# Kernel tuning notes

Measured on AMD Instinct MI355X. Metric: run time of the kernel, lower is better.

## Reference

```python
import jax, jax.numpy as jnp
import numpy as np
from jax import lax

NUM_HEADS = 8
BN_EPS = 1e-5


def setup_inputs() -> dict:
    key = jax.random.key(0)
    ks = jax.random.split(key, 11)
    B, C, H, W = 4, 256, 48, 48
    return {
        "Vx": jax.random.normal(ks[0], (B, C, H, W), jnp.float32),
        "conv_w": jax.random.normal(ks[1], (C, C, 3, 3), jnp.float32) * 0.02,
        "conv_b": jax.random.normal(ks[2], (C,), jnp.float32) * 0.02,
        "bn_gamma": jax.random.uniform(ks[3], (C,), jnp.float32, 0.5, 1.5),
        "bn_beta": jax.random.normal(ks[4], (C,), jnp.float32) * 0.02,
        "bn_mean": jax.random.normal(ks[5], (C,), jnp.float32) * 0.02,
        "bn_var": jax.random.uniform(ks[6], (C,), jnp.float32, 0.5, 1.5),
        "qkv_w": jax.random.normal(ks[7], (3 * C, C), jnp.float32) * 0.02,
        "qkv_b": jax.random.normal(ks[8], (3 * C,), jnp.float32) * 0.02,
        "proj_w": jax.random.normal(ks[9], (C, C), jnp.float32) * 0.02,
        "proj_b": jax.random.normal(ks[10], (C,), jnp.float32) * 0.02,
    }


def reference(Vx, conv_w, conv_b, bn_gamma, bn_beta, bn_mean, bn_var,
              qkv_w, qkv_b, proj_w, proj_b):
    # 3x3 conv (stride 1, pad 1) + BN (inference) + ReLU
    x = lax.conv_general_dilated(
        Vx, conv_w, window_strides=(1, 1), padding='SAME',
        dimension_numbers=('NCHW', 'OIHW', 'NCHW'))
    x = x + conv_b[None, :, None, None]
    inv = bn_gamma * lax.rsqrt(bn_var + BN_EPS)
    x = x * inv[None, :, None, None] + (bn_beta - bn_mean * inv)[None, :, None, None]
    x = jax.nn.relu(x)

    B, C, H, W = x.shape
    N = H * W
    h = NUM_HEADS
    d = C // h
    scale = float(d) ** -0.5  # (dim / num_heads) ** -0.5

    # 1x1 qkv conv == channel matmul; faithful interleaved per-head split:
    # reshape(B, h, 3d, N) then chunk along dim 2
    qkv = jnp.einsum('oc,bchw->bohw', qkv_w, x) + qkv_b[None, :, None, None]
    qkv = qkv.reshape(B, h, 3 * d, N)
    q, k, v = qkv[:, :, :d], qkv[:, :, d:2 * d], qkv[:, :, 2 * d:]

    # attn[b,h,n,m] = sum_d q[b,h,d,n] k[b,h,d,m] * scale ; softmax over m
    attn = jax.nn.softmax(jnp.einsum('bhdn,bhdm->bhnm', q, k) * scale, axis=-1)
    # out = value @ attn^T : out[b,h,e,n] = sum_m v[b,h,e,m] attn[b,h,n,m]
    out = jnp.einsum('bhem,bhnm->bhen', v, attn).reshape(B, C, H, W)

    # 1x1 proj conv
    out = jnp.einsum('oc,bchw->bohw', proj_w, out) + proj_b[None, :, None, None]
    return out
```

## Files before the change

### kernel.cpp

```cpp
#include <hip/hip_runtime.h>
#include <math.h>

#define BB 4
#define CCH 256
#define NSP 2304
#define NHEAD 8
#define DH 32

typedef __bf16 bf16x8 __attribute__((ext_vector_type(8)));
typedef float f32x16 __attribute__((ext_vector_type(16)));
typedef unsigned u32x2 __attribute__((ext_vector_type(2)));
typedef unsigned u32x4 __attribute__((ext_vector_type(4)));

static __device__ __forceinline__ unsigned cvtpk(float lo, float hi) {
  unsigned r;
  asm("v_cvt_pk_bf16_f32 %0, %1, %2" : "=v"(r) : "v"(lo), "v"(hi));
  return r;
}

#if __has_builtin(__builtin_amdgcn_exp2f)
static __device__ __forceinline__ float fexp2(float x) { return __builtin_amdgcn_exp2f(x); }
#else
static __device__ __forceinline__ float fexp2(float x) { return exp2f(x); }
#endif

#if __has_builtin(__builtin_amdgcn_rcpf)
static __device__ __forceinline__ float frcp(float x) { return __builtin_amdgcn_rcpf(x); }
#else
static __device__ __forceinline__ float frcp(float x) { return 1.f / x; }
#endif

__global__ __launch_bounds__(256) void k_xt(const float* __restrict__ Vx,
    __bf16* __restrict__ xt)
{
  __shared__ __bf16 Lt[64 * 40];
  int bid = blockIdx.x;
  const int nt = bid % 36; bid /= 36;
  const int cit = bid % 8; const int b = bid / 8;
  const int n0 = nt * 64, ci0 = cit * 32;
  const int tid = threadIdx.x;
  {
    const int ci = tid >> 3, ns = (tid & 7) * 8;
    const float* src = Vx + ((size_t)(b * CCH + ci0 + ci)) * NSP + n0 + ns;
    float4 v0 = *(const float4*)src;
    float4 v1 = *(const float4*)(src + 4);
    Lt[(ns+0)*40 + ci] = (__bf16)v0.x;  Lt[(ns+1)*40 + ci] = (__bf16)v0.y;
    Lt[(ns+2)*40 + ci] = (__bf16)v0.z;  Lt[(ns+3)*40 + ci] = (__bf16)v0.w;
    Lt[(ns+4)*40 + ci] = (__bf16)v1.x;  Lt[(ns+5)*40 + ci] = (__bf16)v1.y;
    Lt[(ns+6)*40 + ci] = (__bf16)v1.z;  Lt[(ns+7)*40 + ci] = (__bf16)v1.w;
  }
  __syncthreads();
  {
    const int n = tid >> 2, cip = (tid & 3) * 8;
    bf16x8 r = *(bf16x8*)&Lt[n * 40 + cip];
    *(bf16x8*)&xt[((size_t)b * NSP + n0 + n) * CCH + ci0 + cip] = r;
  }
}

__global__ __launch_bounds__(256) void k_wt(const float* __restrict__ cw,
    __bf16* __restrict__ wt)
{
  const int co = blockIdx.x, ci = threadIdx.x;
  const float* rd = cw + ((size_t)co * CCH + ci) * 9;
#pragma unroll
  for (int p = 0; p < 9; ++p)
    wt[((size_t)p * CCH + co) * CCH + ci] = (__bf16)rd[p];
}

#define XLP 40

__global__ __launch_bounds__(256) void k_conv_mfma(const __bf16* __restrict__ xt,
    const __bf16* __restrict__ wt,
    const float* __restrict__ cb, const float* __restrict__ g,
    const float* __restrict__ be, const float* __restrict__ mu,
    const float* __restrict__ va, __bf16* __restrict__ xq)
{
  __shared__ __bf16 Xl[300 * XLP];
  __shared__ __bf16 Wl[9 * 64 * XLP];
  __shared__ float bn[64][2];
  int bid = blockIdx.x;
  const int nt = bid % 18; bid /= 18;
  const int cot = bid % 4; const int b = bid / 4;
  const int n0 = nt * 128, co0 = cot * 64;
  const int tid = threadIdx.x;
  const int w = tid >> 6, l = tid & 63, h = l >> 5, q = l & 31;
  const int ybase0 = n0 / 48;
  const int y0b = ybase0 - 1;

  if (tid < 64) {
    const int co = co0 + tid;
    const float inv = g[co] * rsqrtf(va[co] + 1e-5f);
    bn[tid][0] = inv;
    bn[tid][1] = (cb[co] - mu[co]) * inv + be[co];
  }

  const int nabs = n0 + w * 32 + q;
  const int yab = nabs / 48, xab = nabs - yab * 48;
  const int sb = (yab - ybase0) * 50 + xab;

  const __bf16* xtb = xt + (size_t)b * NSP * CCH;

  f32x16 acc0, acc1;
#pragma unroll
  for (int r = 0; r < 16; ++r) { acc0[r] = 0.f; acc1[r] = 0.f; }

  for (int cc = 0; cc < 8; ++cc) {
    __syncthreads();
#pragma unroll
    for (int it = 0; it < 5; ++it) {
      const int v = it * 256 + tid;
      if (v < 1200) {
        const int sp = v >> 2, cip = (v & 3) * 8;
        const int r = sp / 50, xp = sp - r * 50;
        const int gy = y0b + r, gx = xp - 1;
        bf16x8 val;
#pragma unroll
        for (int j = 0; j < 8; ++j) val[j] = (__bf16)0.f;
        if ((unsigned)gy < 48u && (unsigned)gx < 48u)
          val = *(const bf16x8*)&xtb[(size_t)(gy * 48 + gx) * CCH + cc * 32 + cip];
        *(bf16x8*)&Xl[sp * XLP + cip] = val;
      }
    }
    {
      const int co = tid >> 2, cip = (tid & 3) * 8;
      const __bf16* wsrc = wt + (size_t)(co0 + co) * CCH + cc * 32 + cip;
#pragma unroll
      for (int p = 0; p < 9; ++p) {
        bf16x8 wv = *(const bf16x8*)&wsrc[(size_t)p * CCH * CCH];
        *(bf16x8*)&Wl[(p * 64 + co) * XLP + cip] = wv;
      }
    }
    __syncthreads();
#pragma unroll
    for (int p = 0; p < 9; ++p) {
      const int dy = p / 3, dx = p - 3 * (p / 3);
#pragma unroll
      for (int ks = 0; ks < 2; ++ks) {
        bf16x8 a0 = *(bf16x8*)&Wl[(p * 64 + q) * XLP + ks * 16 + 8 * h];
        bf16x8 a1 = *(bf16x8*)&Wl[(p * 64 + 32 + q) * XLP + ks * 16 + 8 * h];
        bf16x8 bf = *(bf16x8*)&Xl[(sb + dy * 50 + dx) * XLP + ks * 16 + 8 * h];
        acc0 = __builtin_amdgcn_mfma_f32_32x32x16_bf16(a0, bf, acc0, 0, 0, 0);
        acc1 = __builtin_amdgcn_mfma_f32_32x32x16_bf16(a1, bf, acc1, 0, 0, 0);
      }
    }
  }

  __bf16* op = xq + ((size_t)b * NSP + nabs) * CCH + co0;
#pragma unroll
  for (int gg = 0; gg < 4; ++gg) {
    const int cl0 = 8 * gg + 4 * h;
    float v0 = fmaxf(fmaf(acc0[4*gg+0], bn[cl0+0][0], bn[cl0+0][1]), 0.f);
    float v1 = fmaxf(fmaf(acc0[4*gg+1], bn[cl0+1][0], bn[cl0+1][1]), 0.f);
    float v2 = fmaxf(fmaf(acc0[4*gg+2], bn[cl0+2][0], bn[cl0+2][1]), 0.f);
    float v3 = fmaxf(fmaf(acc0[4*gg+3], bn[cl0+3][0], bn[cl0+3][1]), 0.f);
    u32x2 pk; pk[0] = cvtpk(v0, v1); pk[1] = cvtpk(v2, v3);
    *(u32x2*)&op[cl0] = pk;
    float w0 = fmaxf(fmaf(acc1[4*gg+0], bn[32+cl0+0][0], bn[32+cl0+0][1]), 0.f);
    float w1 = fmaxf(fmaf(acc1[4*gg+1], bn[32+cl0+1][0], bn[32+cl0+1][1]), 0.f);
    float w2 = fmaxf(fmaf(acc1[4*gg+2], bn[32+cl0+2][0], bn[32+cl0+2][1]), 0.f);
    float w3 = fmaxf(fmaf(acc1[4*gg+3], bn[32+cl0+3][0], bn[32+cl0+3][1]), 0.f);
    u32x2 qk; qk[0] = cvtpk(w0, w1); qk[1] = cvtpk(w2, w3);
    *(u32x2*)&op[32 + cl0] = qk;
  }
}

__global__ __launch_bounds__(256) void k_gemm_mfma(const __bf16* __restrict__ X,
    const float* __restrict__ Wm, const float* __restrict__ bias,
    __bf16* __restrict__ Y)
{
  __shared__ __bf16 Xl[128 * XLP];
  __shared__ __bf16 Wl[64 * XLP];
  const int tid = threadIdx.x;
  int bid = blockIdx.x;
  const int nt = bid % 18; bid /= 18;
  const int ot = bid % 12; const int b = bid / 12;
  const int o0 = ot * 64, n0 = nt * 128;
  const int w = tid >> 6, l = tid & 63, h = l >> 5, q = l & 31;

  const int xrow = tid >> 1, xcip = (tid & 1) * 16;
  const int wrow = tid >> 2, wcip = (tid & 3) * 8;
  const __bf16* Xb = X + (size_t)b * NSP * CCH + (size_t)(n0 + xrow) * CCH;

  f32x16 acc0, acc1;
#pragma unroll
  for (int r = 0; r < 16; ++r) { acc0[r] = 0.f; acc1[r] = 0.f; }

  bf16x8 xa0, xa1; float4 wa0, wa1;
  xa0 = *(const bf16x8*)&Xb[xcip];
  xa1 = *(const bf16x8*)&Xb[xcip + 8];
  wa0 = *(const float4*)&Wm[(size_t)(o0 + wrow) * CCH + wcip];
  wa1 = *(const float4*)&Wm[(size_t)(o0 + wrow) * CCH + wcip + 4];

  for (int cc = 0; cc < 8; ++cc) {
    __syncthreads();
    *(bf16x8*)&Xl[xrow * XLP + xcip]     = xa0;
    *(bf16x8*)&Xl[xrow * XLP + xcip + 8] = xa1;
    {
      bf16x8 wv;
      wv[0]=(__bf16)wa0.x; wv[1]=(__bf16)wa0.y; wv[2]=(__bf16)wa0.z; wv[3]=(__bf16)wa0.w;
      wv[4]=(__bf16)wa1.x; wv[5]=(__bf16)wa1.y; wv[6]=(__bf16)wa1.z; wv[7]=(__bf16)wa1.w;
      *(bf16x8*)&Wl[wrow * XLP + wcip] = wv;
    }
    __syncthreads();
    if (cc < 7) {
      const int c1 = (cc + 1) * 32;
      xa0 = *(const bf16x8*)&Xb[c1 + xcip];
      xa1 = *(const bf16x8*)&Xb[c1 + xcip + 8];
      wa0 = *(const float4*)&Wm[(size_t)(o0 + wrow) * CCH + c1 + wcip];
      wa1 = *(const float4*)&Wm[(size_t)(o0 + wrow) * CCH + c1 + wcip + 4];
    }
#pragma unroll
    for (int ks = 0; ks < 2; ++ks) {
      bf16x8 a0 = *(bf16x8*)&Wl[q * XLP + ks * 16 + 8 * h];
      bf16x8 a1 = *(bf16x8*)&Wl[(32 + q) * XLP + ks * 16 + 8 * h];
      bf16x8 bfr = *(bf16x8*)&Xl[(w * 32 + q) * XLP + ks * 16 + 8 * h];
      acc0 = __builtin_amdgcn_mfma_f32_32x32x16_bf16(a0, bfr, acc0, 0, 0, 0);
      acc1 = __builtin_amdgcn_mfma_f32_32x32x16_bf16(a1, bfr, acc1, 0, 0, 0);
    }
  }

  const int n = n0 + w * 32 + q;
  const float QS = 1.4426950408889634f * 0.17677669529663687f;
#pragma unroll
  for (int j = 0; j < 2; ++j) {
    const int t = 2 * ot + j;
    const int head = t / 3, comp = t - 3 * (t / 3);
    const float sc = (comp == 0) ? QS : 1.0f;
    __bf16* yb = Y + (((size_t)(b * NHEAD + head) * 3 + comp) * NSP + n) * DH;
    const f32x16& A = j ? acc1 : acc0;
#pragma unroll
    for (int gg = 0; gg < 4; ++gg) {
      const int e0 = 8 * gg + 4 * h;
      const int ob = o0 + 32 * j + e0;
      u32x2 pk;
      pk[0] = cvtpk((A[4*gg+0] + bias[ob+0]) * sc, (A[4*gg+1] + bias[ob+1]) * sc);
      pk[1] = cvtpk((A[4*gg+2] + bias[ob+2]) * sc, (A[4*gg+3] + bias[ob+3]) * sc);
      *(u32x2*)&yb[e0] = pk;
    }
  }
}

#define KLS 40
#define VLS 72
#define NSPLIT 4
#define NST 9

__global__ __launch_bounds__(256) void k_attn_mfma(const __bf16* __restrict__ qkvt,
    __bf16* __restrict__ parts, float* __restrict__ rss)
{
  __shared__ __bf16 K_lds[2][64 * KLS];
  __shared__ __bf16 Vt_lds[2][32 * VLS];
  const int tid = threadIdx.x;
  const int bid0 = blockIdx.x;
  const int bid = (bid0 & 7) * 288 + (bid0 >> 3);
  const int bh  = bid / 72;
  const int rem = bid % 72;
  const int qb  = rem >> 2;
  const int ks  = rem & 3;
  const int w  = tid >> 6;
  const int l  = tid & 63;
  const int h  = l >> 5;
  const int q  = l & 31;

  const __bf16* qg = qkvt + ((size_t)bh * 3    ) * NSP * DH;
  const __bf16* kg = qkvt + ((size_t)bh * 3 + 1) * NSP * DH;
  const __bf16* vg = qkvt + ((size_t)bh * 3 + 2) * NSP * DH;

  const int nq = qb * 128 + w * 32 + q;
  bf16x8 qf0 = *(const bf16x8*)&qg[(size_t)nq * DH + 8 * h];
  bf16x8 qf1 = *(const bf16x8*)&qg[(size_t)nq * DH + 16 + 8 * h];

  f32x16 zf;
#pragma unroll
  for (int r = 0; r < 16; ++r) zf[r] = 0.f;
  bf16x8 onesA;
#pragma unroll
  for (int j = 0; j < 8; ++j) onesA[j] = (__bf16)1.0f;

  f32x16 acc0, acc1, rsacc;
#pragma unroll
  for (int r = 0; r < 16; ++r) { acc0[r] = 0.f; acc1[r] = 0.f; rsacc[r] = 0.f; }

  const int krow = tid >> 2, kcol = (tid & 3) * 8;
  const int vrow = tid & 63, vcol = (tid >> 6) * 8;
  const int m0 = ks * (NST * 64);

  bf16x8 ka = *(const bf16x8*)&kg[(size_t)(m0 + krow) * DH + kcol];
  bf16x8 va = *(const bf16x8*)&vg[(size_t)(m0 + vrow) * DH + vcol];
  *(bf16x8*)&K_lds[0][krow * KLS + kcol] = ka;
#pragma unroll
  for (int j = 0; j < 8; ++j) Vt_lds[0][(vcol + j) * VLS + vrow] = va[j];
  ka = *(const bf16x8*)&kg[(size_t)(m0 + 64 + krow) * DH + kcol];
  va = *(const bf16x8*)&vg[(size_t)(m0 + 64 + vrow) * DH + vcol];
  __syncthreads();

  for (int s = 0; s < NST; ++s) {
    const int cur = s & 1;
    if (s + 1 < NST) {
      *(bf16x8*)&K_lds[cur ^ 1][krow * KLS + kcol] = ka;
#pragma unroll
      for (int j = 0; j < 8; ++j) Vt_lds[cur ^ 1][(vcol + j) * VLS + vrow] = va[j];
      if (s + 2 < NST) {
        const int m2 = m0 + (s + 2) * 64;
        ka = *(const bf16x8*)&kg[(size_t)(m2 + krow) * DH + kcol];
        va = *(const bf16x8*)&vg[(size_t)(m2 + vrow) * DH + vcol];
      }
    }
    __builtin_amdgcn_s_setprio(1);
#pragma unroll
    for (int kt = 0; kt < 2; ++kt) {
      bf16x8 kfr0 = *(bf16x8*)&K_lds[cur][(32*kt + q) * KLS + 8*h];
      bf16x8 kfr1 = *(bf16x8*)&K_lds[cur][(32*kt + q) * KLS + 16 + 8*h];
      f32x16 sv;
      sv = __builtin_amdgcn_mfma_f32_32x32x16_bf16(kfr0, qf0, zf, 0, 0, 0);
      sv = __builtin_amdgcn_mfma_f32_32x32x16_bf16(kfr1, qf1, sv, 0, 0, 0);
      float p[16];
#pragma unroll
      for (int r = 0; r < 16; ++r) p[r] = fexp2(sv[r]);
#pragma unroll
      for (int m = 0; m < 2; ++m) {
        unsigned pk00 = cvtpk(p[8*m+0], p[8*m+1]);
        unsigned pk01 = cvtpk(p[8*m+2], p[8*m+3]);
        unsigned pk10 = cvtpk(p[8*m+4], p[8*m+5]);
        unsigned pk11 = cvtpk(p[8*m+6], p[8*m+7]);
        asm("v_permlane32_swap_b32 %0, %1" : "+v"(pk00), "+v"(pk10));
        asm("v_permlane32_swap_b32 %0, %1" : "+v"(pk01), "+v"(pk11));
        u32x4 pw = {pk00, pk01, pk10, pk11};
        bf16x8 pfr = __builtin_bit_cast(bf16x8, pw);
        const int MT = 2*kt + m;
        bf16x8 vfr = *(bf16x8*)&Vt_lds[cur][q * VLS + 16*MT + 8*h];
        if (MT & 1) acc1 = __builtin_amdgcn_mfma_f32_32x32x16_bf16(vfr, pfr, acc1, 0, 0, 0);
        else        acc0 = __builtin_amdgcn_mfma_f32_32x32x16_bf16(vfr, pfr, acc0, 0, 0, 0);
        rsacc = __builtin_amdgcn_mfma_f32_32x32x16_bf16(onesA, pfr, rsacc, 0, 0, 0);
      }
    }
    __builtin_amdgcn_s_setprio(0);
    __syncthreads();
  }

  const int b = bh >> 3, head = bh & 7;
  __bf16* ob = parts + (size_t)ks * 2359296
             + ((size_t)b * NSP + nq) * CCH + head * DH;
#pragma unroll
  for (int gg = 0; gg < 4; ++gg) {
    const int e0 = 8 * gg + 4 * h;
    u32x2 pk;
    pk[0] = cvtpk(acc0[4*gg+0] + acc1[4*gg+0], acc0[4*gg+1] + acc1[4*gg+1]);
    pk[1] = cvtpk(acc0[4*gg+2] + acc1[4*gg+2], acc0[4*gg+3] + acc1[4*gg+3]);
    *(u32x2*)&ob[e0] = pk;
  }
  if (h == 0)
    rss[(size_t)ks * 73728 + (size_t)bh * NSP + nq] = rsacc[0];
}

__global__ __launch_bounds__(256) void k_proj_mfma(const __bf16* __restrict__ parts,
    const float* __restrict__ rss, const float* __restrict__ Wm,
    const float* __restrict__ bias, float* __restrict__ Y)
{
  __shared__ __bf16 Xl[128 * XLP];
  __shared__ __bf16 Wl[64 * XLP];
  const int tid = threadIdx.x;
  int bid = blockIdx.x;
  const int nt = bid % 18; bid /= 18;
  const int ot = bid % 4; const int b = bid / 4;
  const int o0 = ot * 64, n0 = nt * 128;
  const int w = tid >> 6, l = tid & 63, h = l >> 5, q = l & 31;

  const int xrow = tid >> 1, xcip = (tid & 1) * 16;
  const int wrow = tid >> 2, wcip = (tid & 3) * 8;
  const int nrow = n0 + xrow;
  const size_t xbase = ((size_t)b * NSP + nrow) * CCH + xcip;
  const size_t rbase = (size_t)(b * NHEAD) * NSP + nrow;

  f32x16 acc0, acc1;
#pragma unroll
  for (int r = 0; r < 16; ++r) { acc0[r] = 0.f; acc1[r] = 0.f; }

  bf16x8 pa[4], pb[4]; float rs4[4]; float4 wa0, wa1;
#pragma unroll
  for (int ksp = 0; ksp < 4; ++ksp) {
    pa[ksp] = *(const bf16x8*)&parts[(size_t)ksp * 2359296 + xbase];
    pb[ksp] = *(const bf16x8*)&parts[(size_t)ksp * 2359296 + xbase + 8];
    rs4[ksp] = rss[(size_t)ksp * 73728 + rbase];
  }
  wa0 = *(const float4*)&Wm[(size_t)(o0 + wrow) * CCH + wcip];
  wa1 = *(const float4*)&Wm[(size_t)(o0 + wrow) * CCH + wcip + 4];

  for (int cc = 0; cc < 8; ++cc) {
    __syncthreads();
    {
      const float rn = frcp(rs4[0] + rs4[1] + rs4[2] + rs4[3]);
      float s0[8], s1[8];
#pragma unroll
      for (int j = 0; j < 8; ++j) {
        s0[j] = ((float)pa[0][j] + (float)pa[1][j] + (float)pa[2][j] + (float)pa[3][j]) * rn;
        s1[j] = ((float)pb[0][j] + (float)pb[1][j] + (float)pb[2][j] + (float)pb[3][j]) * rn;
      }
      u32x4 o0v, o1v;
#pragma unroll
      for (int j = 0; j < 4; ++j) {
        o0v[j] = cvtpk(s0[2*j], s0[2*j+1]);
        o1v[j] = cvtpk(s1[2*j], s1[2*j+1]);
      }
      *(u32x4*)&Xl[xrow * XLP + xcip]     = o0v;
      *(u32x4*)&Xl[xrow * XLP + xcip + 8] = o1v;
      bf16x8 wv;
      wv[0]=(__bf16)wa0.x; wv[1]=(__bf16)wa0.y; wv[2]=(__bf16)wa0.z; wv[3]=(__bf16)wa0.w;
      wv[4]=(__bf16)wa1.x; wv[5]=(__bf16)wa1.y; wv[6]=(__bf16)wa1.z; wv[7]=(__bf16)wa1.w;
      *(bf16x8*)&Wl[wrow * XLP + wcip] = wv;
    }
    __syncthreads();
    if (cc < 7) {
      const int c1 = (cc + 1) * 32;
#pragma unroll
      for (int ksp = 0; ksp < 4; ++ksp) {
        pa[ksp] = *(const bf16x8*)&parts[(size_t)ksp * 2359296 + xbase + c1];
        pb[ksp] = *(const bf16x8*)&parts[(size_t)ksp * 2359296 + xbase + c1 + 8];
        rs4[ksp] = rss[(size_t)ksp * 73728 + (size_t)(cc + 1) * NSP + rbase];
      }
      wa0 = *(const float4*)&Wm[(size_t)(o0 + wrow) * CCH + c1 + wcip];
      wa1 = *(const float4*)&Wm[(size_t)(o0 + wrow) * CCH + c1 + wcip + 4];
    }
#pragma unroll
    for (int ks = 0; ks < 2; ++ks) {
      bf16x8 a0 = *(bf16x8*)&Wl[q * XLP + ks * 16 + 8 * h];
      bf16x8 a1 = *(bf16x8*)&Wl[(32 + q) * XLP + ks * 16 + 8 * h];
      bf16x8 bfr = *(bf16x8*)&Xl[(w * 32 + q) * XLP + ks * 16 + 8 * h];
      acc0 = __builtin_amdgcn_mfma_f32_32x32x16_bf16(a0, bfr, acc0, 0, 0, 0);
      acc1 = __builtin_amdgcn_mfma_f32_32x32x16_bf16(a1, bfr, acc1, 0, 0, 0);
    }
  }

  const int n = n0 + w * 32 + q;
#pragma unroll
  for (int j = 0; j < 2; ++j) {
    const f32x16& A = j ? acc1 : acc0;
#pragma unroll
    for (int r = 0; r < 16; ++r) {
      const int e = (r & 3) + 8 * (r >> 2) + 4 * h;
      const int o = o0 + 32 * j + e;
      Y[((size_t)b * CCH + o) * NSP + n] = A[r] + bias[o];
    }
  }
}

extern "C" void kernel_launch(void* const* d_in, const int* in_sizes, int n_in,
                              void* d_out, int out_size, void* d_ws, size_t ws_size,
                              hipStream_t stream)
{
  const float* Vx = (const float*)d_in[0];
  const float* cw = (const float*)d_in[1];
  const float* cb = (const float*)d_in[2];
  const float* g  = (const float*)d_in[3];
  const float* be = (const float*)d_in[4];
  const float* mu = (const float*)d_in[5];
  const float* va = (const float*)d_in[6];
  const float* qw = (const float*)d_in[7];
  const float* qb = (const float*)d_in[8];
  const float* pw = (const float*)d_in[9];
  const float* pb = (const float*)d_in[10];
  float* out = (float*)d_out;

  __bf16* xq    = (__bf16*)d_ws;
  __bf16* qkvt  = (__bf16*)((char*)d_ws + 4718592);
  __bf16* parts = (__bf16*)((char*)d_ws + 18874368);
  float*  rss   = (float*) ((char*)d_ws + 37748736);

  __bf16* xt = (__bf16*)d_out;
  __bf16* wt = (__bf16*)((char*)d_out + 4718592);

  k_xt<<<1152, 256, 0, stream>>>(Vx, xt);
  k_wt<<<256, 256, 0, stream>>>(cw, wt);
  k_conv_mfma<<<288, 256, 0, stream>>>(xt, wt, cb, g, be, mu, va, xq);
  k_gemm_mfma<<<4*12*18, 256, 0, stream>>>(xq, qw, qb, qkvt);
  k_attn_mfma<<<2304, 256, 0, stream>>>(qkvt, parts, rss);
  k_proj_mfma<<<4*4*18, 256, 0, stream>>>(parts, rss, pw, pb, out);
}
```

Baseline: 113.7 us.

## Merge prep kernels, shrink conv tiles, and raise attention key split to six

The input transpose and weight conversion kernels become one launch, removing a kernel boundary. The conv kernel now uses 96-pixel by 32-channel tiles with 192 threads and 768 blocks, replacing 288 blocks, to fill more compute units. Attention splits keys six ways instead of four, giving 3456 blocks, and the projection kernel sums six partial results. This adds more partial-result traffic and more redundant halo and weight loads per conv block in exchange for higher occupancy.

New measurement: 115.5 us. No clear change (+1.6%).

```diff
diff --git a/kernel.cpp b/kernel.cpp
--- a/kernel.cpp
+++ b/kernel.cpp
@@ -30,64 +30,61 @@
 static __device__ __forceinline__ float frcp(float x) { return 1.f / x; }
 #endif
 
-__global__ __launch_bounds__(256) void k_xt(const float* __restrict__ Vx,
-    __bf16* __restrict__ xt)
+__global__ __launch_bounds__(256) void k_pre(const float* __restrict__ Vx,
+    const float* __restrict__ cw, __bf16* __restrict__ xt, __bf16* __restrict__ wtb)
 {
   __shared__ __bf16 Lt[64 * 40];
-  int bid = blockIdx.x;
-  const int nt = bid % 36; bid /= 36;
-  const int cit = bid % 8; const int b = bid / 8;
-  const int n0 = nt * 64, ci0 = cit * 32;
   const int tid = threadIdx.x;
-  {
-    const int ci = tid >> 3, ns = (tid & 7) * 8;
-    const float* src = Vx + ((size_t)(b * CCH + ci0 + ci)) * NSP + n0 + ns;
-    float4 v0 = *(const float4*)src;
-    float4 v1 = *(const float4*)(src + 4);
-    Lt[(ns+0)*40 + ci] = (__bf16)v0.x;  Lt[(ns+1)*40 + ci] = (__bf16)v0.y;
-    Lt[(ns+2)*40 + ci] = (__bf16)v0.z;  Lt[(ns+3)*40 + ci] = (__bf16)v0.w;
-    Lt[(ns+4)*40 + ci] = (__bf16)v1.x;  Lt[(ns+5)*40 + ci] = (__bf16)v1.y;
-    Lt[(ns+6)*40 + ci] = (__bf16)v1.z;  Lt[(ns+7)*40 + ci] = (__bf16)v1.w;
-  }
-  __syncthreads();
-  {
-    const int n = tid >> 2, cip = (tid & 3) * 8;
-    bf16x8 r = *(bf16x8*)&Lt[n * 40 + cip];
-    *(bf16x8*)&xt[((size_t)b * NSP + n0 + n) * CCH + ci0 + cip] = r;
-  }
-}
-
-__global__ __launch_bounds__(256) void k_wt(const float* __restrict__ cw,
-    __bf16* __restrict__ wt)
-{
-  const int co = blockIdx.x, ci = threadIdx.x;
-  const float* rd = cw + ((size_t)co * CCH + ci) * 9;
-#pragma unroll
-  for (int p = 0; p < 9; ++p)
-    wt[((size_t)p * CCH + co) * CCH + ci] = (__bf16)rd[p];
+  if (blockIdx.x < 1152) {
+    int bid = blockIdx.x;
+    const int nt = bid % 36; bid /= 36;
+    const int cit = bid % 8; const int b = bid / 8;
+    const int n0 = nt * 64, ci0 = cit * 32;
+    {
+      const int ci = tid >> 3, ns = (tid & 7) * 8;
+      const float* src = Vx + ((size_t)(b * CCH + ci0 + ci)) * NSP + n0 + ns;
+      float4 v0 = *(const float4*)src;
+      float4 v1 = *(const float4*)(src + 4);
+      Lt[(ns+0)*40 + ci] = (__bf16)v0.x;  Lt[(ns+1)*40 + ci] = (__bf16)v0.y;
+      Lt[(ns+2)*40 + ci] = (__bf16)v0.z;  Lt[(ns+3)*40 + ci] = (__bf16)v0.w;
+      Lt[(ns+4)*40 + ci] = (__bf16)v1.x;  Lt[(ns+5)*40 + ci] = (__bf16)v1.y;
+      Lt[(ns+6)*40 + ci] = (__bf16)v1.z;  Lt[(ns+7)*40 + ci] = (__bf16)v1.w;
+    }
+    __syncthreads();
+    {
+      const int n = tid >> 2, cip = (tid & 3) * 8;
+      bf16x8 r = *(bf16x8*)&Lt[n * 40 + cip];
+      *(bf16x8*)&xt[((size_t)b * NSP + n0 + n) * CCH + ci0 + cip] = r;
+    }
+  } else {
+    const int co = blockIdx.x - 1152, ci = tid;
+    const float* rd = cw + ((size_t)co * CCH + ci) * 9;
+#pragma unroll
+    for (int p = 0; p < 9; ++p)
+      wtb[((size_t)p * CCH + co) * CCH + ci] = (__bf16)rd[p];
+  }
 }
 
 #define XLP 40
 
-__global__ __launch_bounds__(256) void k_conv_mfma(const __bf16* __restrict__ xt,
+__global__ __launch_bounds__(192) void k_conv_mfma(const __bf16* __restrict__ xt,
     const __bf16* __restrict__ wt,
     const float* __restrict__ cb, const float* __restrict__ g,
     const float* __restrict__ be, const float* __restrict__ mu,
     const float* __restrict__ va, __bf16* __restrict__ xq)
 {
-  __shared__ __bf16 Xl[300 * XLP];
-  __shared__ __bf16 Wl[9 * 64 * XLP];
-  __shared__ float bn[64][2];
-  int bid = blockIdx.x;
-  const int nt = bid % 18; bid /= 18;
-  const int cot = bid % 4; const int b = bid / 4;
-  const int n0 = nt * 128, co0 = cot * 64;
+  __shared__ __bf16 Xl[200 * XLP];
+  __shared__ __bf16 Wl[9 * 32 * XLP];
+  __shared__ float bn[32][2];
+  const int bid0 = blockIdx.x;
+  int bid = (bid0 & 7) * 96 + (bid0 >> 3);
+  const int nt = bid % 24; bid /= 24;
+  const int cot = bid % 8; const int b = bid / 8;
+  const int n0 = nt * 96, co0 = cot * 32, row0 = nt * 2;
   const int tid = threadIdx.x;
   const int w = tid >> 6, l = tid & 63, h = l >> 5, q = l & 31;
-  const int ybase0 = n0 / 48;
-  const int y0b = ybase0 - 1;
-
-  if (tid < 64) {
+
+  if (tid < 32) {
     const int co = co0 + tid;
     const float inv = g[co] * rsqrtf(va[co] + 1e-5f);
     bn[tid][0] = inv;
@@ -96,23 +93,23 @@
 
   const int nabs = n0 + w * 32 + q;
   const int yab = nabs / 48, xab = nabs - yab * 48;
-  const int sb = (yab - ybase0) * 50 + xab;
+  const int sb = (yab - row0) * 50 + xab;
 
   const __bf16* xtb = xt + (size_t)b * NSP * CCH;
 
-  f32x16 acc0, acc1;
-#pragma unroll
-  for (int r = 0; r < 16; ++r) { acc0[r] = 0.f; acc1[r] = 0.f; }
+  f32x16 acc;
+#pragma unroll
+  for (int r = 0; r < 16; ++r) acc[r] = 0.f;
 
   for (int cc = 0; cc < 8; ++cc) {
     __syncthreads();
 #pragma unroll
     for (int it = 0; it < 5; ++it) {
-      const int v = it * 256 + tid;
-      if (v < 1200) {
+      const int v = it * 192 + tid;
+      if (v < 800) {
         const int sp = v >> 2, cip = (v & 3) * 8;
         const int r = sp / 50, xp = sp - r * 50;
-        const int gy = y0b + r, gx = xp - 1;
+        const int gy = row0 - 1 + r, gx = xp - 1;
         bf16x8 val;
 #pragma unroll
         for (int j = 0; j < 8; ++j) val[j] = (__bf16)0.f;
@@ -121,14 +118,13 @@
         *(bf16x8*)&Xl[sp * XLP + cip] = val;
       }
     }
-    {
+    if (tid < 128) {
       const int co = tid >> 2, cip = (tid & 3) * 8;
       const __bf16* wsrc = wt + (size_t)(co0 + co) * CCH + cc * 32 + cip;
 #pragma unroll
-      for (int p = 0; p < 9; ++p) {
-        bf16x8 wv = *(const bf16x8*)&wsrc[(size_t)p * CCH * CCH];
-        *(bf16x8*)&Wl[(p * 64 + co) * XLP + cip] = wv;
-      }
+      for (int p = 0; p < 9; ++p)
+        *(bf16x8*)&Wl[(p * 32 + co) * XLP + cip] =
+            *(const bf16x8*)&wsrc[(size_t)p * CCH * CCH];
     }
     __syncthreads();
 #pragma unroll
@@ -136,11 +132,9 @@
       const int dy = p / 3, dx = p - 3 * (p / 3);
 #pragma unroll
       for (int ks = 0; ks < 2; ++ks) {
-        bf16x8 a0 = *(bf16x8*)&Wl[(p * 64 + q) * XLP + ks * 16 + 8 * h];
-        bf16x8 a1 = *(bf16x8*)&Wl[(p * 64 + 32 + q) * XLP + ks * 16 + 8 * h];
+        bf16x8 a  = *(bf16x8*)&Wl[(p * 32 + q) * XLP + ks * 16 + 8 * h];
         bf16x8 bf = *(bf16x8*)&Xl[(sb + dy * 50 + dx) * XLP + ks * 16 + 8 * h];
-        acc0 = __builtin_amdgcn_mfma_f32_32x32x16_bf16(a0, bf, acc0, 0, 0, 0);
-        acc1 = __builtin_amdgcn_mfma_f32_32x32x16_bf16(a1, bf, acc1, 0, 0, 0);
+        acc = __builtin_amdgcn_mfma_f32_32x32x16_bf16(a, bf, acc, 0, 0, 0);
       }
     }
   }
@@ -149,18 +143,12 @@
 #pragma unroll
   for (int gg = 0; gg < 4; ++gg) {
     const int cl0 = 8 * gg + 4 * h;
-    float v0 = fmaxf(fmaf(acc0[4*gg+0], bn[cl0+0][0], bn[cl0+0][1]), 0.f);
-    float v1 = fmaxf(fmaf(acc0[4*gg+1], bn[cl0+1][0], bn[cl0+1][1]), 0.f);
-    float v2 = fmaxf(fmaf(acc0[4*gg+2], bn[cl0+2][0], bn[cl0+2][1]), 0.f);
-    float v3 = fmaxf(fmaf(acc0[4*gg+3], bn[cl0+3][0], bn[cl0+3][1]), 0.f);
+    float v0 = fmaxf(fmaf(acc[4*gg+0], bn[cl0+0][0], bn[cl0+0][1]), 0.f);
+    float v1 = fmaxf(fmaf(acc[4*gg+1], bn[cl0+1][0], bn[cl0+1][1]), 0.f);
+    float v2 = fmaxf(fmaf(acc[4*gg+2], bn[cl0+2][0], bn[cl0+2][1]), 0.f);
+    float v3 = fmaxf(fmaf(acc[4*gg+3], bn[cl0+3][0], bn[cl0+3][1]), 0.f);
     u32x2 pk; pk[0] = cvtpk(v0, v1); pk[1] = cvtpk(v2, v3);
     *(u32x2*)&op[cl0] = pk;
-    float w0 = fmaxf(fmaf(acc1[4*gg+0], bn[32+cl0+0][0], bn[32+cl0+0][1]), 0.f);
-    float w1 = fmaxf(fmaf(acc1[4*gg+1], bn[32+cl0+1][0], bn[32+cl0+1][1]), 0.f);
-    float w2 = fmaxf(fmaf(acc1[4*gg+2], bn[32+cl0+2][0], bn[32+cl0+2][1]), 0.f);
-    float w3 = fmaxf(fmaf(acc1[4*gg+3], bn[32+cl0+3][0], bn[32+cl0+3][1]), 0.f);
-    u32x2 qk; qk[0] = cvtpk(w0, w1); qk[1] = cvtpk(w2, w3);
-    *(u32x2*)&op[32 + cl0] = qk;
   }
 }
 
@@ -242,8 +230,8 @@
 
 #define KLS 40
 #define VLS 72
-#define NSPLIT 4
-#define NST 9
+#define NSPLIT 6
+#define NST 6
 
 __global__ __launch_bounds__(256) void k_attn_mfma(const __bf16* __restrict__ qkvt,
     __bf16* __restrict__ parts, float* __restrict__ rss)
@@ -252,11 +240,11 @@
   __shared__ __bf16 Vt_lds[2][32 * VLS];
   const int tid = threadIdx.x;
   const int bid0 = blockIdx.x;
-  const int bid = (bid0 & 7) * 288 + (bid0 >> 3);
-  const int bh  = bid / 72;
-  const int rem = bid % 72;
-  const int qb  = rem >> 2;
-  const int ks  = rem & 3;
+  const int bid = (bid0 & 7) * 432 + (bid0 >> 3);
+  const int bh  = bid / 108;
+  const int rem = bid % 108;
+  const int qb  = rem / NSPLIT;
+  const int ks  = rem % NSPLIT;
   const int w  = tid >> 6;
   const int l  = tid & 63;
   const int h  = l >> 5;
@@ -376,12 +364,12 @@
 #pragma unroll
   for (int r = 0; r < 16; ++r) { acc0[r] = 0.f; acc1[r] = 0.f; }
 
-  bf16x8 pa[4], pb[4]; float rs4[4]; float4 wa0, wa1;
-#pragma unroll
-  for (int ksp = 0; ksp < 4; ++ksp) {
+  bf16x8 pa[NSPLIT], pb[NSPLIT]; float rs6[NSPLIT]; float4 wa0, wa1;
+#pragma unroll
+  for (int ksp = 0; ksp < NSPLIT; ++ksp) {
     pa[ksp] = *(const bf16x8*)&parts[(size_t)ksp * 2359296 + xbase];
     pb[ksp] = *(const bf16x8*)&parts[(size_t)ksp * 2359296 + xbase + 8];
-    rs4[ksp] = rss[(size_t)ksp * 73728 + rbase];
+    rs6[ksp] = rss[(size_t)ksp * 73728 + rbase];
   }
   wa0 = *(const float4*)&Wm[(size_t)(o0 + wrow) * CCH + wcip];
   wa1 = *(const float4*)&Wm[(size_t)(o0 + wrow) * CCH + wcip + 4];
@@ -389,12 +377,19 @@
   for (int cc = 0; cc < 8; ++cc) {
     __syncthreads();
     {
-      const float rn = frcp(rs4[0] + rs4[1] + rs4[2] + rs4[3]);
+      float rsum = rs6[0];
+#pragma unroll
+      for (int ksp = 1; ksp < NSPLIT; ++ksp) rsum += rs6[ksp];
+      const float rn = frcp(rsum);
       float s0[8], s1[8];
 #pragma unroll
       for (int j = 0; j < 8; ++j) {
-        s0[j] = ((float)pa[0][j] + (float)pa[1][j] + (float)pa[2][j] + (float)pa[3][j]) * rn;
-        s1[j] = ((float)pb[0][j] + (float)pb[1][j] + (float)pb[2][j] + (float)pb[3][j]) * rn;
+        float a = (float)pa[0][j], bsum = (float)pb[0][j];
+#pragma unroll
+        for (int ksp = 1; ksp < NSPLIT; ++ksp) {
+          a += (float)pa[ksp][j]; bsum += (float)pb[ksp][j];
+        }
+        s0[j] = a * rn; s1[j] = bsum * rn;
       }
       u32x4 o0v, o1v;
 #pragma unroll
@@ -413,10 +408,10 @@
     if (cc < 7) {
       const int c1 = (cc + 1) * 32;
 #pragma unroll
-      for (int ksp = 0; ksp < 4; ++ksp) {
+      for (int ksp = 0; ksp < NSPLIT; ++ksp) {
         pa[ksp] = *(const bf16x8*)&parts[(size_t)ksp * 2359296 + xbase + c1];
         pb[ksp] = *(const bf16x8*)&parts[(size_t)ksp * 2359296 + xbase + c1 + 8];
-        rs4[ksp] = rss[(size_t)ksp * 73728 + (size_t)(cc + 1) * NSP + rbase];
+        rs6[ksp] = rss[(size_t)ksp * 73728 + (size_t)(cc + 1) * NSP + rbase];
       }
       wa0 = *(const float4*)&Wm[(size_t)(o0 + wrow) * CCH + c1 + wcip];
       wa1 = *(const float4*)&Wm[(size_t)(o0 + wrow) * CCH + c1 + wcip + 4];
@@ -464,15 +459,14 @@
   __bf16* xq    = (__bf16*)d_ws;
   __bf16* qkvt  = (__bf16*)((char*)d_ws + 4718592);
   __bf16* parts = (__bf16*)((char*)d_ws + 18874368);
-  float*  rss   = (float*) ((char*)d_ws + 37748736);
+  float*  rss   = (float*) ((char*)d_ws + 47185920);
 
   __bf16* xt = (__bf16*)d_out;
   __bf16* wt = (__bf16*)((char*)d_out + 4718592);
 
-  k_xt<<<1152, 256, 0, stream>>>(Vx, xt);
-  k_wt<<<256, 256, 0, stream>>>(cw, wt);
-  k_conv_mfma<<<288, 256, 0, stream>>>(xt, wt, cb, g, be, mu, va, xq);
+  k_pre<<<1408, 256, 0, stream>>>(Vx, cw, xt, wt);
+  k_conv_mfma<<<768, 192, 0, stream>>>(xt, wt, cb, g, be, mu, va, xq);
   k_gemm_mfma<<<4*12*18, 256, 0, stream>>>(xq, qw, qb, qkvt);
-  k_attn_mfma<<<2304, 256, 0, stream>>>(qkvt, parts, rss);
+  k_attn_mfma<<<3456, 256, 0, stream>>>(qkvt, parts, rss);
   k_proj_mfma<<<4*4*18, 256, 0, stream>>>(parts, rss, pw, pb, out);
 }
```
